# Optimization experiments

Hardware: AMD Instinct MI355X
Metric: run time of the kernel (lower is better)

Reference implementation:

```python
import jax, jax.numpy as jnp
import numpy as np

B = 256        # graph pairs
MAX_SET = 64   # nodes per graph == max_set_size (padding is identity)
E = 512        # edges per graph
D = 128        # node_state_dim == av.filters_3
T = 64         # av.transform_dim
N_PROP = 5
N_TIME = 3
TEMP = 0.1
SINK_ITERS = 20
NG = 2 * B
N = NG * MAX_SET
TOT_E = NG * E


def sinkhorn(log_alpha):
    la = log_alpha / TEMP
    for _ in range(SINK_ITERS):
        la = la - jax.nn.logsumexp(la, axis=2, keepdims=True)
        la = la - jax.nn.logsumexp(la, axis=1, keepdims=True)
    return jnp.exp(la)


def setup_inputs() -> dict:
    key = jax.random.key(0)
    ks = jax.random.split(key, 32)

    def lin(k, i, o):
        return jax.random.normal(k, (i, o), jnp.float32) / np.sqrt(i).astype(np.float32)

    node_features = jax.random.normal(ks[0], (N, 32), jnp.float32)
    edge_features = jax.random.normal(ks[1], (TOT_E, 16), jnp.float32)
    offs = jnp.repeat(jnp.arange(NG, dtype=jnp.int32) * MAX_SET, E)
    from_idx = jax.random.randint(ks[2], (TOT_E,), 0, MAX_SET, jnp.int32) + offs
    to_idx = jax.random.randint(ks[3], (TOT_E,), 0, MAX_SET, jnp.int32) + offs
    return {
        "node_features": node_features, "edge_features": edge_features,
        "from_idx": from_idx, "to_idx": to_idx,
        "node_enc_w": lin(ks[4], 32, D), "node_enc_b": jnp.zeros((D,), jnp.float32),
        "edge_enc_w": lin(ks[5], 16, 64), "edge_enc_b": jnp.zeros((64,), jnp.float32),
        "mw1": lin(ks[6], 2 * D + 64, 2 * D), "mb1": jnp.zeros((2 * D,), jnp.float32),
        "mw2": lin(ks[7], 2 * D, D), "mb2": jnp.zeros((D,), jnp.float32),
        "nw1": lin(ks[8], 2 * D, 2 * D), "nb1": jnp.zeros((2 * D,), jnp.float32),
        "nw2": lin(ks[9], 2 * D, D), "nb2": jnp.zeros((D,), jnp.float32),
        "cw1": lin(ks[10], 2 * D, 2 * D), "cb1": jnp.zeros((2 * D,), jnp.float32),
        "cw2": lin(ks[11], 2 * D, D), "cb2": jnp.zeros((D,), jnp.float32),
        "t1w": lin(ks[12], D, T), "t1b": jnp.zeros((T,), jnp.float32),
        "t2w": lin(ks[13], T, T), "t2b": jnp.zeros((T,), jnp.float32),
    }


def reference(node_features, edge_features, from_idx, to_idx,
              node_enc_w, node_enc_b, edge_enc_w, edge_enc_b,
              mw1, mb1, mw2, mb2, nw1, nb1, nw2, nb2,
              cw1, cb1, cw2, cb2, t1w, t1b, t2w, t2b):
    # Encoder (GMN GraphEncoder: linear maps on raw node/edge features)
    h0 = node_features @ node_enc_w + node_enc_b          # [N, D]
    e0 = edge_features @ edge_enc_w + edge_enc_b          # [TOT_E, 64]
    store = jnp.zeros((N, D * (N_PROP + 1)), h0.dtype)    # node_feature_store
    plan = None
    for _t in range(N_TIME):
        h = h0
        parts = [jnp.zeros((N, D), h0.dtype)]             # slot 0 stays zero
        for p in range(1, N_PROP + 1):
            inter = store[:, (p - 1) * D: p * D]          # time_update_idx == 'k_t'
            comb = jax.nn.relu(jnp.concatenate([h, inter], 1) @ cw1 + cb1) @ cw2 + cb2
            # GraphPropLayer: gather -> message MLP -> segment_sum -> node update MLP
            msg_in = jnp.concatenate([comb[from_idx], comb[to_idx], e0], 1)
            messages = jax.nn.relu(msg_in @ mw1 + mb1) @ mw2 + mb2
            agg = jax.ops.segment_sum(messages, to_idx, num_segments=N)
            h = jax.nn.relu(jnp.concatenate([comb, agg], 1) @ nw1 + nb1) @ nw2 + nb2
            parts.append(h)
        store = jnp.concatenate(parts, 1)                 # [N, D*(K+1)]
        # split into padded query/corpus stacks (all graphs have MAX_SET nodes,
        # so F.pad and the size masks are identity here)
        s = store.reshape(NG, MAX_SET, -1)
        q, c = s[0::2], s[1::2]                           # [B, M, D*(K+1)]
        tq = jax.nn.relu(q[:, :, -D:] @ t1w + t1b) @ t2w + t2b
        tc = jax.nn.relu(c[:, :, -D:] @ t1w + t1b) @ t2w + t2b
        sim = jnp.einsum('bqt,bct->bqc', tq, tc)
        plan = sinkhorn(sim)                              # node transport plan [B,M,M]
        qfc = jnp.einsum('bqc,bcd->bqd', plan, c)
        cfq = jnp.einsum('bqc,bqd->bcd', plan, q)
        inter_feats = jnp.stack([qfc, cfq], 1)[:, :, :, D:].reshape(N, N_PROP * D)
        store = store.at[:, D:].set(inter_feats)
    return plan
```

## Files before the change

kernel.cpp:

```cpp
#include <hip/hip_runtime.h>
#include <hip/hip_bf16.h>

#define NNODES   32768
#define NGROUPS  512
#define EPG      512
#define ND       (32768l*128)

typedef __attribute__((ext_vector_type(4))) float f32x4;
typedef __attribute__((ext_vector_type(8))) short bf16x8;

__device__ __forceinline__ short f2bf(float x) {
  unsigned u = __float_as_uint(x);
  unsigned r = (u + 0x7FFF + ((u >> 16) & 1)) >> 16;
  return (short)r;
}
__device__ __forceinline__ float bf2f(short h) {
  return __uint_as_float(((unsigned)(unsigned short)h) << 16);
}
__device__ __forceinline__ void split3(float x, short* ph, short* pm, short* pl, long idx) {
  short h = f2bf(x); float r1 = x - bf2f(h);
  short m = f2bf(r1); float r2 = r1 - bf2f(m);
  ph[idx] = h; pm[idx] = m; pl[idx] = f2bf(r2);
}

__global__ void k_node_enc(const float* __restrict__ nf, const float* __restrict__ w,
                           const float* __restrict__ b, float* __restrict__ h0) {
  int idx = blockIdx.x * 256 + threadIdx.x;
  int row = idx >> 7, col = idx & 127;
  const float* x = nf + row * 32;
  float acc = b[col];
#pragma unroll
  for (int k = 0; k < 32; ++k) acc = fmaf(x[k], w[k * 128 + col], acc);
  h0[idx] = acc;
}

__global__ void k_prep(const float* __restrict__ eew, const float* __restrict__ eeb,
                       const float* __restrict__ mw1, const float* __restrict__ mb1,
                       const float* __restrict__ mb2, const float* __restrict__ nw1,
                       float* __restrict__ Wfold, float* __restrict__ bfold,
                       float* __restrict__ vbias) {
  const int c = threadIdx.x, b = blockIdx.x;
  if (b < 16) {
    float a = 0.f;
    for (int j = 0; j < 64; ++j) a = fmaf(eew[b * 64 + j], mw1[(256 + j) * 256 + c], a);
    Wfold[b * 256 + c] = a;
  } else if (b == 16) {
    float a = mb1[c];
    for (int j = 0; j < 64; ++j) a = fmaf(eeb[j], mw1[(256 + j) * 256 + c], a);
    bfold[c] = a;
  } else {
    float a = 0.f;
    for (int j = 0; j < 128; ++j) a = fmaf(mb2[j], nw1[(128 + j) * 256 + c], a);
    vbias[c] = a;
  }
}

__global__ void k_wsplit3(const float* __restrict__ W, int C, int Kd,
                          short* __restrict__ th, short* __restrict__ tm,
                          short* __restrict__ tl) {
  const int c = blockIdx.x;
  for (int k = threadIdx.x; k < Kd; k += 256) {
    float w = W[(long)k * C + c];
    split3(w, th, tm, tl, c * 256 + k);
  }
}

__global__ void k_csr(const int* __restrict__ from_idx, const int* __restrict__ to_idx,
                      const float* __restrict__ ef,
                      int* __restrict__ csr_f, int* __restrict__ rp_g,
                      float* __restrict__ efp, int* __restrict__ deg) {
  __shared__ int cnt[64], rps[65];
  __shared__ int tls[EPG], fls[EPG];
  __shared__ short ord[EPG];
  const int g = blockIdx.x, tid = threadIdx.x;
  const int be = g * EPG, bn = g * 64;
  if (tid < 64) cnt[tid] = 0;
  __syncthreads();
  for (int e = tid; e < EPG; e += 256) {
    int t = to_idx[be + e] - bn;
    tls[e] = t;
    fls[e] = from_idx[be + e] - bn;
    atomicAdd(&cnt[t], 1);
  }
  __syncthreads();
  if (tid == 0) {
    int s = 0;
    for (int i = 0; i < 64; ++i) { rps[i] = s; s += cnt[i]; }
    rps[64] = s;
  }
  __syncthreads();
  if (tid < 64) {
    int pos = rps[tid];
    for (int e = 0; e < EPG; ++e)
      if (tls[e] == tid) ord[pos++] = (short)e;
  }
  __syncthreads();
  for (int ec = tid; ec < EPG; ec += 256) {
    const int eo = ord[ec];
    csr_f[be + ec] = fls[eo];
    const float4* src = (const float4*)&ef[(long)(be + eo) * 16];
    float4* dst = (float4*)&efp[(long)(be + ec) * 16];
    dst[0] = src[0]; dst[1] = src[1]; dst[2] = src[2]; dst[3] = src[3];
  }
  if (tid < 65) rp_g[g * 65 + tid] = rps[tid];
  if (tid < 64) deg[bn + tid] = cnt[tid];
}

template<int KTOT, bool DEG, bool RPX0, bool WPOUT>
__global__ __launch_bounds__(256, 3)
void k_mlp2m(const float* __restrict__ x0,
             const short* __restrict__ x0h, const short* __restrict__ x0m,
             const short* __restrict__ x0l,
             const float* __restrict__ x1,
             const short* __restrict__ W1h, const short* __restrict__ W1m,
             const short* __restrict__ W1l,
             const float* __restrict__ b1, const int* __restrict__ deg,
             const float* __restrict__ vbias,
             const short* __restrict__ W2h, const short* __restrict__ W2m,
             const short* __restrict__ W2l,
             const float* __restrict__ b2,
             float* __restrict__ out,
             short* __restrict__ outh, short* __restrict__ outm,
             short* __restrict__ outl) {
  __shared__ short xh[32 * 264];
  __shared__ short xm[32 * 264];
  __shared__ short xl[32 * 264];
  __shared__ int degs[32];
  const int tid = threadIdx.x;
  const long row0 = (long)blockIdx.x * 32;

  if constexpr (RPX0) {
    for (int i = tid; i < 32 * 16; i += 256) {
      const int r = i >> 4, q = i & 15;
      const long gb = (row0 + r) * 128 + q * 8;
      const int lb = r * 264 + q * 8;
      *(bf16x8*)&xh[lb] = *(const bf16x8*)&x0h[gb];
      *(bf16x8*)&xm[lb] = *(const bf16x8*)&x0m[gb];
      *(bf16x8*)&xl[lb] = *(const bf16x8*)&x0l[gb];
    }
  } else {
    for (int i = tid; i < 32 * 32; i += 256) {
      const int r = i >> 5, q = i & 31;
      float4 v = *(const float4*)&x0[(row0 + r) * 128 + q * 4];
      const int base = r * 264 + q * 4;
      split3(v.x, xh, xm, xl, base + 0);
      split3(v.y, xh, xm, xl, base + 1);
      split3(v.z, xh, xm, xl, base + 2);
      split3(v.w, xh, xm, xl, base + 3);
    }
  }
  if constexpr (KTOT == 256) {
    for (int i = tid; i < 32 * 32; i += 256) {
      const int r = i >> 5, q = i & 31;
      float4 v = *(const float4*)&x1[(row0 + r) * 128 + q * 4];
      const int base = r * 264 + 128 + q * 4;
      split3(v.x, xh, xm, xl, base + 0);
      split3(v.y, xh, xm, xl, base + 1);
      split3(v.z, xh, xm, xl, base + 2);
      split3(v.w, xh, xm, xl, base + 3);
    }
  }
  if constexpr (DEG) { if (tid < 32) degs[tid] = deg[row0 + tid]; }
  __syncthreads();

  const int lane = tid & 63, wid = tid >> 6;
  const int lr = lane & 15;
  const int lk = (lane >> 4) * 8;
  const int rsub = (lane >> 4) * 4;

  f32x4 acc[2][4];
#pragma unroll
  for (int fc = 0; fc < 4; ++fc) {
    const int col = wid * 64 + fc * 16 + lr;
    const float bv = b1[col];
#pragma unroll
    for (int fr = 0; fr < 2; ++fr) acc[fr][fc] = {bv, bv, bv, bv};
    if constexpr (DEG) {
      const float vb = vbias[col];
#pragma unroll
      for (int fr = 0; fr < 2; ++fr)
#pragma unroll
        for (int r = 0; r < 4; ++r)
          acc[fr][fc][r] += (float)degs[fr * 16 + rsub + r] * vb;
    }
  }

#pragma unroll 2
  for (int ks = 0; ks < KTOT / 32; ++ks) {
    const int k0 = ks * 32 + lk;
    bf16x8 ah[2], am[2], al[2];
#pragma unroll
    for (int fr = 0; fr < 2; ++fr) {
      const int ab = (fr * 16 + lr) * 264 + k0;
      ah[fr] = *(const bf16x8*)&xh[ab];
      am[fr] = *(const bf16x8*)&xm[ab];
      al[fr] = *(const bf16x8*)&xl[ab];
    }
#pragma unroll
    for (int fc = 0; fc < 4; ++fc) {
      const long wrow = (long)(wid * 64 + fc * 16 + lr) * 256 + k0;
      const bf16x8 bh = *(const bf16x8*)&W1h[wrow];
      const bf16x8 bm = *(const bf16x8*)&W1m[wrow];
      const bf16x8 bl = *(const bf16x8*)&W1l[wrow];
#pragma unroll
      for (int fr = 0; fr < 2; ++fr) {
        acc[fr][fc] = __builtin_amdgcn_mfma_f32_16x16x32_bf16(ah[fr], bh, acc[fr][fc], 0, 0, 0);
        acc[fr][fc] = __builtin_amdgcn_mfma_f32_16x16x32_bf16(ah[fr], bm, acc[fr][fc], 0, 0, 0);
        acc[fr][fc] = __builtin_amdgcn_mfma_f32_16x16x32_bf16(am[fr], bh, acc[fr][fc], 0, 0, 0);
        acc[fr][fc] = __builtin_amdgcn_mfma_f32_16x16x32_bf16(ah[fr], bl, acc[fr][fc], 0, 0, 0);
        acc[fr][fc] = __builtin_amdgcn_mfma_f32_16x16x32_bf16(am[fr], bm, acc[fr][fc], 0, 0, 0);
        acc[fr][fc] = __builtin_amdgcn_mfma_f32_16x16x32_bf16(al[fr], bh, acc[fr][fc], 0, 0, 0);
      }
    }
  }
  __syncthreads();

#pragma unroll
  for (int fr = 0; fr < 2; ++fr)
#pragma unroll
    for (int fc = 0; fc < 4; ++fc) {
      const int col = wid * 64 + fc * 16 + lr;
#pragma unroll
      for (int r = 0; r < 4; ++r) {
        const int row = fr * 16 + rsub + r;
        float v = fmaxf(acc[fr][fc][r], 0.f);
        split3(v, xh, xm, xl, row * 264 + col);
      }
    }
  __syncthreads();

  f32x4 acc2[2][2];
#pragma unroll
  for (int fc = 0; fc < 2; ++fc) {
    const float bv = b2[wid * 32 + fc * 16 + lr];
#pragma unroll
    for (int fr = 0; fr < 2; ++fr) acc2[fr][fc] = {bv, bv, bv, bv};
  }
#pragma unroll 2
  for (int ks = 0; ks < 8; ++ks) {
    const int k0 = ks * 32 + lk;
    bf16x8 ah[2], am[2], al[2];
#pragma unroll
    for (int fr = 0; fr < 2; ++fr) {
      const int ab = (fr * 16 + lr) * 264 + k0;
      ah[fr] = *(const bf16x8*)&xh[ab];
      am[fr] = *(const bf16x8*)&xm[ab];
      al[fr] = *(const bf16x8*)&xl[ab];
    }
#pragma unroll
    for (int fc = 0; fc < 2; ++fc) {
      const long wrow = (long)(wid * 32 + fc * 16 + lr) * 256 + k0;
      const bf16x8 bh = *(const bf16x8*)&W2h[wrow];
      const bf16x8 bm = *(const bf16x8*)&W2m[wrow];
      const bf16x8 bl = *(const bf16x8*)&W2l[wrow];
#pragma unroll
      for (int fr = 0; fr < 2; ++fr) {
        acc2[fr][fc] = __builtin_amdgcn_mfma_f32_16x16x32_bf16(ah[fr], bh, acc2[fr][fc], 0, 0, 0);
        acc2[fr][fc] = __builtin_amdgcn_mfma_f32_16x16x32_bf16(ah[fr], bm, acc2[fr][fc], 0, 0, 0);
        acc2[fr][fc] = __builtin_amdgcn_mfma_f32_16x16x32_bf16(am[fr], bh, acc2[fr][fc], 0, 0, 0);
        acc2[fr][fc] = __builtin_amdgcn_mfma_f32_16x16x32_bf16(ah[fr], bl, acc2[fr][fc], 0, 0, 0);
        acc2[fr][fc] = __builtin_amdgcn_mfma_f32_16x16x32_bf16(am[fr], bm, acc2[fr][fc], 0, 0, 0);
        acc2[fr][fc] = __builtin_amdgcn_mfma_f32_16x16x32_bf16(al[fr], bh, acc2[fr][fc], 0, 0, 0);
      }
    }
  }
#pragma unroll
  for (int fr = 0; fr < 2; ++fr)
#pragma unroll
    for (int fc = 0; fc < 2; ++fc) {
      const int col = wid * 32 + fc * 16 + lr;
#pragma unroll
      for (int r = 0; r < 4; ++r) {
        const long gi = (row0 + fr * 16 + rsub + r) * 128 + col;
        if constexpr (WPOUT) {
          split3(acc2[fr][fc][r], outh, outm, outl, gi);
        } else {
          out[gi] = acc2[fr][fc][r];
        }
      }
    }
}

__global__ __launch_bounds__(256, 3)
void k_edgeb(const short* __restrict__ chp, const short* __restrict__ cmp,
             const short* __restrict__ clp,
             const float* __restrict__ efp,
             const short* __restrict__ m1h, const short* __restrict__ m1m,
             const short* __restrict__ m1l,
             const float* __restrict__ Wfold, const float* __restrict__ bfold,
             const int* __restrict__ csr_f, const int* __restrict__ rp_g,
             float* __restrict__ ag) {
  __shared__ __align__(16) float cAB[2 * 64 * 68];
  __shared__ short fl[EPG];
  __shared__ int rp[65];
  float* cA = cAB;
  float* cB = cAB + 64 * 68;

  const int tid = threadIdx.x;
  const int g = blockIdx.x, cb = blockIdx.y;
  const int be = g * EPG, bn = g * 64;
  const int col0 = cb * 64;

  for (int i = tid; i < EPG; i += 256) fl[i] = (short)csr_f[be + i];
  if (tid < 65) rp[tid] = rp_g[g * 65 + tid];

  const int lane = tid & 63, wid = tid >> 6;
  const int lr = lane & 15;
  const int lk = (lane >> 4) * 8;
  const int rsub = (lane >> 4) * 4;
  const int ng = tid >> 4, cg = tid & 15;
  const int n0 = ng * 4, cq = cg * 4;

  {
    const int isB = wid >> 1;
    const int cw = (wid & 1) * 32;
    const int wkof = isB * 128;
    float* dstC = isB ? cB : cA;
#pragma unroll 1
    for (int hf = 0; hf < 2; ++hf) {
      f32x4 c[2][2];
#pragma unroll
      for (int fr = 0; fr < 2; ++fr)
#pragma unroll
        for (int fc = 0; fc < 2; ++fc) c[fr][fc] = {0.f, 0.f, 0.f, 0.f};
      for (int ks = 0; ks < 4; ++ks) {
        const int k0 = ks * 32 + lk;
        bf16x8 ah[2], am[2], al[2];
#pragma unroll
        for (int fr = 0; fr < 2; ++fr) {
          const long ga = (long)(bn + (hf * 2 + fr) * 16 + lr) * 128 + k0;
          ah[fr] = *(const bf16x8*)&chp[ga];
          am[fr] = *(const bf16x8*)&cmp[ga];
          al[fr] = *(const bf16x8*)&clp[ga];
        }
#pragma unroll
        for (int fc = 0; fc < 2; ++fc) {
          const long wrow = (long)(col0 + cw + fc * 16 + lr) * 256 + wkof + k0;
          const bf16x8 bh = *(const bf16x8*)&m1h[wrow];
          const bf16x8 bm = *(const bf16x8*)&m1m[wrow];
          const bf16x8 bl = *(const bf16x8*)&m1l[wrow];
#pragma unroll
          for (int fr = 0; fr < 2; ++fr) {
            c[fr][fc] = __builtin_amdgcn_mfma_f32_16x16x32_bf16(ah[fr], bh, c[fr][fc], 0, 0, 0);
            c[fr][fc] = __builtin_amdgcn_mfma_f32_16x16x32_bf16(ah[fr], bm, c[fr][fc], 0, 0, 0);
            c[fr][fc] = __builtin_amdgcn_mfma_f32_16x16x32_bf16(am[fr], bh, c[fr][fc], 0, 0, 0);
            c[fr][fc] = __builtin_amdgcn_mfma_f32_16x16x32_bf16(ah[fr], bl, c[fr][fc], 0, 0, 0);
            c[fr][fc] = __builtin_amdgcn_mfma_f32_16x16x32_bf16(am[fr], bm, c[fr][fc], 0, 0, 0);
            c[fr][fc] = __builtin_amdgcn_mfma_f32_16x16x32_bf16(al[fr], bh, c[fr][fc], 0, 0, 0);
          }
        }
      }
#pragma unroll
      for (int fr = 0; fr < 2; ++fr)
#pragma unroll
        for (int fc = 0; fc < 2; ++fc) {
          const int col = cw + fc * 16 + lr;
#pragma unroll
          for (int r = 0; r < 4; ++r)
            dstC[((hf * 2 + fr) * 16 + rsub + r) * 68 + col] = c[fr][fc][r];
        }
    }
  }
  float4 Wf[16];
#pragma unroll
  for (int k = 0; k < 16; ++k) Wf[k] = *(const float4*)&Wfold[k * 256 + col0 + cq];
  const float4 bf = *(const float4*)&bfold[col0 + cq];
  __syncthreads();

#pragma unroll
  for (int i = 0; i < 4; ++i) {
    const int n = n0 + i;
    const float4 cBn = *(const float4*)&cB[n * 68 + cq];
    const int eBeg = rp[n], eEnd = rp[n + 1];
    float4 acc0 = make_float4(0.f, 0.f, 0.f, 0.f);
    float4 acc1 = make_float4(0.f, 0.f, 0.f, 0.f);
    int e = eBeg;
    for (; e + 1 < eEnd; e += 2) {
      const int f0 = fl[e], f1 = fl[e + 1];
      const float* er0 = efp + (long)(be + e) * 16;
      const float* er1 = efp + (long)(be + e + 1) * 16;
      float4 ea[4], eb[4];
#pragma unroll
      for (int kq = 0; kq < 4; ++kq) { ea[kq] = ((const float4*)er0)[kq]; eb[kq] = ((const float4*)er1)[kq]; }
      float4 h0 = bf, h1 = bf;
#pragma unroll
      for (int kq = 0; kq < 4; ++kq) {
        const float ev0[4] = {ea[kq].x, ea[kq].y, ea[kq].z, ea[kq].w};
        const float ev1[4] = {eb[kq].x, eb[kq].y, eb[kq].z, eb[kq].w};
#pragma unroll
        for (int s = 0; s < 4; ++s) {
          const float4 w = Wf[kq * 4 + s];
          h0.x = fmaf(ev0[s], w.x, h0.x); h0.y = fmaf(ev0[s], w.y, h0.y);
          h0.z = fmaf(ev0[s], w.z, h0.z); h0.w = fmaf(ev0[s], w.w, h0.w);
          h1.x = fmaf(ev1[s], w.x, h1.x); h1.y = fmaf(ev1[s], w.y, h1.y);
          h1.z = fmaf(ev1[s], w.z, h1.z); h1.w = fmaf(ev1[s], w.w, h1.w);
        }
      }
      const float4 va0 = *(const float4*)&cA[f0 * 68 + cq];
      const float4 va1 = *(const float4*)&cA[f1 * 68 + cq];
      acc0.x += fmaxf(h0.x + va0.x + cBn.x, 0.f);
      acc0.y += fmaxf(h0.y + va0.y + cBn.y, 0.f);
      acc0.z += fmaxf(h0.z + va0.z + cBn.z, 0.f);
      acc0.w += fmaxf(h0.w + va0.w + cBn.w, 0.f);
      acc1.x += fmaxf(h1.x + va1.x + cBn.x, 0.f);
      acc1.y += fmaxf(h1.y + va1.y + cBn.y, 0.f);
      acc1.z += fmaxf(h1.z + va1.z + cBn.z, 0.f);
      acc1.w += fmaxf(h1.w + va1.w + cBn.w, 0.f);
    }
    if (e < eEnd) {
      const int f = fl[e];
      const float* er = efp + (long)(be + e) * 16;
      float4 h = bf;
#pragma unroll
      for (int kq = 0; kq < 4; ++kq) {
        const float4 e4 = ((const float4*)er)[kq];
        const float ev[4] = {e4.x, e4.y, e4.z, e4.w};
#pragma unroll
        for (int s = 0; s < 4; ++s) {
          const float4 w = Wf[kq * 4 + s];
          h.x = fmaf(ev[s], w.x, h.x); h.y = fmaf(ev[s], w.y, h.y);
          h.z = fmaf(ev[s], w.z, h.z); h.w = fmaf(ev[s], w.w, h.w);
        }
      }
      const float4 va = *(const float4*)&cA[f * 68 + cq];
      acc0.x += fmaxf(h.x + va.x + cBn.x, 0.f);
      acc0.y += fmaxf(h.y + va.y + cBn.y, 0.f);
      acc0.z += fmaxf(h.z + va.z + cBn.z, 0.f);
      acc0.w += fmaxf(h.w + va.w + cBn.w, 0.f);
    }
    acc0.x += acc1.x; acc0.y += acc1.y; acc0.z += acc1.z; acc0.w += acc1.w;
    *(float4*)&ag[(long)(bn + n) * 256 + col0 + cq] = acc0;
  }
}

__global__ __launch_bounds__(256, 3)
void k_aggm(const float* __restrict__ ag,
            const short* __restrict__ m2h, const short* __restrict__ m2m,
            const short* __restrict__ m2l, float* __restrict__ aggM) {
  __shared__ short xh[32 * 264];
  __shared__ short xm[32 * 264];
  __shared__ short xl[32 * 264];
  const int tid = threadIdx.x;
  const long row0 = (long)blockIdx.x * 32;

  for (int i = tid; i < 2048; i += 256) {
    const int r = i >> 6, q = i & 63;
    float4 v = *(const float4*)&ag[(row0 + r) * 256 + q * 4];
    const int base = r * 264 + q * 4;
    split3(v.x, xh, xm, xl, base + 0);
    split3(v.y, xh, xm, xl, base + 1);
    split3(v.z, xh, xm, xl, base + 2);
    split3(v.w, xh, xm, xl, base + 3);
  }
  __syncthreads();

  const int lane = tid & 63, wid = tid >> 6;
  const int lr = lane & 15;
  const int lk = (lane >> 4) * 8;
  const int rsub = (lane >> 4) * 4;

  f32x4 s0[2][2], s1[2][2];
#pragma unroll
  for (int fc = 0; fc < 2; ++fc)
#pragma unroll
    for (int fr = 0; fr < 2; ++fr) { s0[fr][fc] = {0.f, 0.f, 0.f, 0.f}; s1[fr][fc] = {0.f, 0.f, 0.f, 0.f}; }

#pragma unroll 2
  for (int ks = 0; ks < 4; ++ks) {
    const int k0 = ks * 32 + lk;
    bf16x8 ah[2], am[2], al[2];
#pragma unroll
    for (int fr = 0; fr < 2; ++fr) {
      const int ab = (fr * 16 + lr) * 264 + k0;
      ah[fr] = *(const bf16x8*)&xh[ab];
      am[fr] = *(const bf16x8*)&xm[ab];
      al[fr] = *(const bf16x8*)&xl[ab];
    }
#pragma unroll
    for (int fc = 0; fc < 2; ++fc) {
      const long wrow = (long)(wid * 32 + fc * 16 + lr) * 256 + k0;
      const bf16x8 bh = *(const bf16x8*)&m2h[wrow];
      const bf16x8 bm = *(const bf16x8*)&m2m[wrow];
      const bf16x8 bl = *(const bf16x8*)&m2l[wrow];
#pragma unroll
      for (int fr = 0; fr < 2; ++fr) {
        s0[fr][fc] = __builtin_amdgcn_mfma_f32_16x16x32_bf16(ah[fr], bh, s0[fr][fc], 0, 0, 0);
        s0[fr][fc] = __builtin_amdgcn_mfma_f32_16x16x32_bf16(ah[fr], bm, s0[fr][fc], 0, 0, 0);
        s0[fr][fc] = __builtin_amdgcn_mfma_f32_16x16x32_bf16(am[fr], bh, s0[fr][fc], 0, 0, 0);
        s0[fr][fc] = __builtin_amdgcn_mfma_f32_16x16x32_bf16(ah[fr], bl, s0[fr][fc], 0, 0, 0);
        s0[fr][fc] = __builtin_amdgcn_mfma_f32_16x16x32_bf16(am[fr], bm, s0[fr][fc], 0, 0, 0);
        s0[fr][fc] = __builtin_amdgcn_mfma_f32_16x16x32_bf16(al[fr], bh, s0[fr][fc], 0, 0, 0);
      }
    }
  }
#pragma unroll 2
  for (int ks = 4; ks < 8; ++ks) {
    const int k0 = ks * 32 + lk;
    bf16x8 ah[2], am[2], al[2];
#pragma unroll
    for (int fr = 0; fr < 2; ++fr) {
      const int ab = (fr * 16 + lr) * 264 + k0;
      ah[fr] = *(const bf16x8*)&xh[ab];
      am[fr] = *(const bf16x8*)&xm[ab];
      al[fr] = *(const bf16x8*)&xl[ab];
    }
#pragma unroll
    for (int fc = 0; fc < 2; ++fc) {
      const long wrow = (long)(wid * 32 + fc * 16 + lr) * 256 + k0;
      const bf16x8 bh = *(const bf16x8*)&m2h[wrow];
      const bf16x8 bm = *(const bf16x8*)&m2m[wrow];
      const bf16x8 bl = *(const bf16x8*)&m2l[wrow];
#pragma unroll
      for (int fr = 0; fr < 2; ++fr) {
        s1[fr][fc] = __builtin_amdgcn_mfma_f32_16x16x32_bf16(ah[fr], bh, s1[fr][fc], 0, 0, 0);
        s1[fr][fc] = __builtin_amdgcn_mfma_f32_16x16x32_bf16(ah[fr], bm, s1[fr][fc], 0, 0, 0);
        s1[fr][fc] = __builtin_amdgcn_mfma_f32_16x16x32_bf16(am[fr], bh, s1[fr][fc], 0, 0, 0);
        s1[fr][fc] = __builtin_amdgcn_mfma_f32_16x16x32_bf16(ah[fr], bl, s1[fr][fc], 0, 0, 0);
        s1[fr][fc] = __builtin_amdgcn_mfma_f32_16x16x32_bf16(am[fr], bm, s1[fr][fc], 0, 0, 0);
        s1[fr][fc] = __builtin_amdgcn_mfma_f32_16x16x32_bf16(al[fr], bh, s1[fr][fc], 0, 0, 0);
      }
    }
  }
#pragma unroll
  for (int fr = 0; fr < 2; ++fr)
#pragma unroll
    for (int fc = 0; fc < 2; ++fc) {
      const int col = wid * 32 + fc * 16 + lr;
#pragma unroll
      for (int r = 0; r < 4; ++r)
        aggM[(row0 + fr * 16 + rsub + r) * 128 + col] = s0[fr][fc][r] + s1[fr][fc][r];
    }
}

__global__ void k_tfeat(const float* __restrict__ x,
                        const float* __restrict__ t1w, const float* __restrict__ t1b,
                        const float* __restrict__ t2w, const float* __restrict__ t2b,
                        float* __restrict__ tf) {
  __shared__ float xs[4][128];
  __shared__ float ys[4][64];
  const int tid = threadIdx.x;
  const long row0 = (long)blockIdx.x * 4;
  for (int i = tid; i < 512; i += 256)
    xs[i >> 7][i & 127] = x[(row0 + (i >> 7)) * 128 + (i & 127)];
  __syncthreads();
  const int r = tid >> 6, c = tid & 63;
  float acc = t1b[c];
#pragma unroll 4
  for (int k = 0; k < 128; ++k) acc = fmaf(xs[r][k], t1w[k * 64 + c], acc);
  ys[r][c] = fmaxf(acc, 0.f);
  __syncthreads();
  float a2 = t2b[c];
#pragma unroll 4
  for (int k = 0; k < 64; ++k) a2 = fmaf(ys[r][k], t2w[k * 64 + c], a2);
  tf[(row0 + r) * 64 + c] = a2;
}

__global__ void k_sim(const float* __restrict__ tf, float* __restrict__ sim) {
  const int b = blockIdx.x, tid = threadIdx.x;
  __shared__ float tq[64][65];
  __shared__ float tcs[64][65];
  for (int i = tid; i < 4096; i += 256) {
    tq[i >> 6][i & 63]  = tf[(long)b * 8192 + i];
    tcs[i >> 6][i & 63] = tf[(long)b * 8192 + 4096 + i];
  }
  __syncthreads();
  const int m = tid >> 2, j0 = (tid & 3) * 16;
#pragma unroll
  for (int j = 0; j < 16; ++j) {
    float a = 0.f;
#pragma unroll 4
    for (int k = 0; k < 64; ++k) a = fmaf(tq[m][k], tcs[j0 + j][k], a);
    sim[(long)b * 4096 + m * 64 + j0 + j] = a;
  }
}

__global__ void k_sink(float* __restrict__ sim, float* __restrict__ outp) {
  const int b = blockIdx.x, tid = threadIdx.x;
  __shared__ float la[64][65];
  const float C = 14.426950408889634f;
  for (int i = tid; i < 4096; i += 256)
    la[i >> 6][i & 63] = sim[(long)b * 4096 + i] * C;
  __syncthreads();
  const int r4 = tid >> 2, l4 = tid & 3;
  for (int it = 0; it < 20; ++it) {
    {
      float m = -3.4e38f;
#pragma unroll
      for (int i = 0; i < 16; ++i) m = fmaxf(m, la[r4][l4 + 4 * i]);
      m = fmaxf(m, __shfl_xor(m, 1)); m = fmaxf(m, __shfl_xor(m, 2));
      float s = 0.f;
#pragma unroll
      for (int i = 0; i < 16; ++i) s += exp2f(la[r4][l4 + 4 * i] - m);
      s += __shfl_xor(s, 1); s += __shfl_xor(s, 2);
      const float lse = m + log2f(s);
#pragma unroll
      for (int i = 0; i < 16; ++i) la[r4][l4 + 4 * i] -= lse;
    }
    __syncthreads();
    {
      float m = -3.4e38f;
#pragma unroll
      for (int i = 0; i < 16; ++i) m = fmaxf(m, la[l4 + 4 * i][r4]);
      m = fmaxf(m, __shfl_xor(m, 1)); m = fmaxf(m, __shfl_xor(m, 2));
      float s = 0.f;
#pragma unroll
      for (int i = 0; i < 16; ++i) s += exp2f(la[l4 + 4 * i][r4] - m);
      s += __shfl_xor(s, 1); s += __shfl_xor(s, 2);
      const float lse = m + log2f(s);
#pragma unroll
      for (int i = 0; i < 16; ++i) la[l4 + 4 * i][r4] -= lse;
    }
    __syncthreads();
  }
  for (int i = tid; i < 4096; i += 256) {
    const float v = exp2f(la[i >> 6][i & 63]);
    outp[(long)b * 4096 + i] = v;
    sim[(long)b * 4096 + i] = v;
  }
}

__global__ void k_mix(const float* __restrict__ plan, const float* __restrict__ src,
                      float* __restrict__ dst) {
  const int b = blockIdx.x, tid = threadIdx.x;
  __shared__ float pl[64][65];
  __shared__ float qs[64][128];
  __shared__ float cs[64][128];
  const long qbase = (long)(2 * b) * 64, cbase = qbase + 64;
  for (int i = tid; i < 4096; i += 256) pl[i >> 6][i & 63] = plan[(long)b * 4096 + i];
  for (int i = tid; i < 8192; i += 256) {
    qs[i >> 7][i & 127] = src[qbase * 128 + i];
    cs[i >> 7][i & 127] = src[cbase * 128 + i];
  }
  __syncthreads();
  const int d = tid & 127, m0 = (tid >> 7) * 32;
  for (int m = m0; m < m0 + 32; ++m) {
    float a = 0.f;
#pragma unroll 4
    for (int j = 0; j < 64; ++j) a = fmaf(pl[m][j], cs[j][d], a);
    dst[(qbase + m) * 128 + d] = a;
  }
  for (int j = m0; j < m0 + 32; ++j) {
    float a = 0.f;
#pragma unroll 4
    for (int m = 0; m < 64; ++m) a = fmaf(pl[m][j], qs[m][d], a);
    dst[(cbase + j) * 128 + d] = a;
  }
}

extern "C" void kernel_launch(void* const* d_in, const int* in_sizes, int n_in,
                              void* d_out, int out_size, void* d_ws, size_t ws_size,
                              hipStream_t stream) {
  const float* nf  = (const float*)d_in[0];
  const float* ef  = (const float*)d_in[1];
  const int* from_idx = (const int*)d_in[2];
  const int* to_idx   = (const int*)d_in[3];
  const float* new_w = (const float*)d_in[4];
  const float* new_b = (const float*)d_in[5];
  const float* eew = (const float*)d_in[6];
  const float* eeb = (const float*)d_in[7];
  const float* mw1 = (const float*)d_in[8];
  const float* mb1 = (const float*)d_in[9];
  const float* mw2 = (const float*)d_in[10];
  const float* mb2 = (const float*)d_in[11];
  const float* nw1 = (const float*)d_in[12];
  const float* nb1 = (const float*)d_in[13];
  const float* nw2 = (const float*)d_in[14];
  const float* nb2 = (const float*)d_in[15];
  const float* cw1 = (const float*)d_in[16];
  const float* cb1 = (const float*)d_in[17];
  const float* cw2 = (const float*)d_in[18];
  const float* cb2 = (const float*)d_in[19];
  const float* t1w = (const float*)d_in[20];
  const float* t1b = (const float*)d_in[21];
  const float* t2w = (const float*)d_in[22];
  const float* t2b = (const float*)d_in[23];

  float* W = (float*)d_ws;
  float* h0     = W;
  float* aggM0  = h0 + ND;
  float* ag     = aggM0 + ND;
  float* parts  = ag + 2 * ND;
  float* efp    = parts + 5 * ND;
  float* Wfold  = efp + 262144l * 16;
  float* bfold  = Wfold + 4096;
  float* vbias  = bfold + 256;
  int*   deg    = (int*)(vbias + 256);
  int*   csr_f  = deg + 32768;
  int*   rp_g   = csr_f + 262144;
  short* cw1t_h = (short*)(rp_g + 33280);
  short* cw1t_m = cw1t_h + 65536;
  short* cw1t_l = cw1t_m + 65536;
  short* nw1t_h = cw1t_l + 65536;
  short* nw1t_m = nw1t_h + 65536;
  short* nw1t_l = nw1t_m + 65536;
  short* cw2t_h = nw1t_l + 65536;
  short* cw2t_m = cw2t_h + 32768;
  short* cw2t_l = cw2t_m + 32768;
  short* nw2t_h = cw2t_l + 32768;
  short* nw2t_m = nw2t_h + 32768;
  short* nw2t_l = nw2t_m + 32768;
  short* m1t_h  = nw2t_l + 32768;
  short* m1t_m  = m1t_h + 65536;
  short* m1t_l  = m1t_m + 65536;
  short* m2t_h  = m1t_l + 65536;
  short* m2t_m  = m2t_h + 32768;
  short* m2t_l  = m2t_m + 32768;
  short* chp    = m2t_l + 32768;
  short* cmp    = chp + 32768l * 128;
  short* clp    = cmp + 32768l * 128;
  float* tf     = aggM0;
  float* sim    = aggM0 + 2097152;
  float* outp   = (float*)d_out;

  k_prep<<<18, 256, 0, stream>>>(eew, eeb, mw1, mb1, mb2, nw1, Wfold, bfold, vbias);
  k_csr<<<512, 256, 0, stream>>>(from_idx, to_idx, ef, csr_f, rp_g, efp, deg);
  k_wsplit3<<<256, 256, 0, stream>>>(cw1, 256, 256, cw1t_h, cw1t_m, cw1t_l);
  k_wsplit3<<<256, 256, 0, stream>>>(nw1, 256, 256, nw1t_h, nw1t_m, nw1t_l);
  k_wsplit3<<<128, 256, 0, stream>>>(cw2, 128, 256, cw2t_h, cw2t_m, cw2t_l);
  k_wsplit3<<<128, 256, 0, stream>>>(nw2, 128, 256, nw2t_h, nw2t_m, nw2t_l);
  k_wsplit3<<<256, 256, 0, stream>>>(mw1, 256, 256, m1t_h, m1t_m, m1t_l);
  k_wsplit3<<<128, 256, 0, stream>>>(mw2, 128, 256, m2t_h, m2t_m, m2t_l);
  k_node_enc<<<16384, 256, 0, stream>>>(nf, new_w, new_b, h0);

  for (int t = 0; t < 3; ++t) {
    const float* hprev = h0;
    for (int p = 1; p <= 5; ++p) {
      if (t > 0 && p > 1)
        k_mlp2m<256, false, false, true><<<1024, 256, 0, stream>>>(
            hprev, nullptr, nullptr, nullptr,
            parts + (long)(p - 1) * ND,
            cw1t_h, cw1t_m, cw1t_l, cb1, nullptr, nullptr,
            cw2t_h, cw2t_m, cw2t_l, cb2, nullptr, chp, cmp, clp);
      else
        k_mlp2m<128, false, false, true><<<1024, 256, 0, stream>>>(
            hprev, nullptr, nullptr, nullptr, nullptr,
            cw1t_h, cw1t_m, cw1t_l, cb1, nullptr, nullptr,
            cw2t_h, cw2t_m, cw2t_l, cb2, nullptr, chp, cmp, clp);
      k_edgeb<<<dim3(512, 4), 256, 0, stream>>>(chp, cmp, clp, efp,
                                                m1t_h, m1t_m, m1t_l,
                                                Wfold, bfold, csr_f, rp_g, ag);
      k_aggm<<<1024, 256, 0, stream>>>(ag, m2t_h, m2t_m, m2t_l, aggM0);
      float* hnew = parts + (long)(p - 1) * ND;
      k_mlp2m<256, true, true, false><<<1024, 256, 0, stream>>>(
          nullptr, chp, cmp, clp, aggM0,
          nw1t_h, nw1t_m, nw1t_l, nb1, deg, vbias,
          nw2t_h, nw2t_m, nw2t_l, nb2, hnew, nullptr, nullptr, nullptr);
      hprev = hnew;
    }
    k_tfeat<<<8192, 256, 0, stream>>>(parts + 4 * ND, t1w, t1b, t2w, t2b, tf);
    k_sim<<<256, 256, 0, stream>>>(tf, sim);
    k_sink<<<256, 256, 0, stream>>>(sim, outp);
    if (t < 2) {
      for (int pi = 3; pi >= 0; --pi)
        k_mix<<<256, 256, 0, stream>>>(sim, parts + (long)pi * ND, parts + (long)(pi + 1) * ND);
    }
  }
}
```

Before: 5.611 ms.

## Fuse message-aggregate projection into node-update MLP kernel and unroll edge loop by three

The separate k_aggm kernel, which projected the aggregated message sums through mw2, is removed. That projection now runs as a prologue inside the node-update k_mlp2m, whose result is split straight into the shared-memory operand tiles. This drops one launch per propagation step and the global write and read of the 128-wide aggM buffer. Separately, the edge accumulation loop in k_edgeb is unrolled by three instead of two, which adds ILP but raises register pressure; the fused kernel also uses more registers and runs longer per block.

```diff
diff --git a/kernel.cpp b/kernel.cpp
--- a/kernel.cpp
+++ b/kernel.cpp
@@ -106,12 +106,14 @@
   if (tid < 64) deg[bn + tid] = cnt[tid];
 }
 
-template<int KTOT, bool DEG, bool RPX0, bool WPOUT>
+template<int KTOT, bool DEG, bool RPX0, bool WPOUT, bool AGG>
 __global__ __launch_bounds__(256, 3)
 void k_mlp2m(const float* __restrict__ x0,
              const short* __restrict__ x0h, const short* __restrict__ x0m,
              const short* __restrict__ x0l,
              const float* __restrict__ x1,
+             const short* __restrict__ A2h, const short* __restrict__ A2m,
+             const short* __restrict__ A2l,
              const short* __restrict__ W1h, const short* __restrict__ W1m,
              const short* __restrict__ W1l,
              const float* __restrict__ b1, const int* __restrict__ deg,
@@ -129,6 +131,100 @@
   const int tid = threadIdx.x;
   const long row0 = (long)blockIdx.x * 32;
 
+  const int lane = tid & 63, wid = tid >> 6;
+  const int lr = lane & 15;
+  const int lk = (lane >> 4) * 8;
+  const int rsub = (lane >> 4) * 4;
+
+  if constexpr (AGG) {
+    for (int i = tid; i < 2048; i += 256) {
+      const int r = i >> 6, q = i & 63;
+      float4 v = *(const float4*)&x1[(row0 + r) * 256 + q * 4];
+      const int base = r * 264 + q * 4;
+      split3(v.x, xh, xm, xl, base + 0);
+      split3(v.y, xh, xm, xl, base + 1);
+      split3(v.z, xh, xm, xl, base + 2);
+      split3(v.w, xh, xm, xl, base + 3);
+    }
+    __syncthreads();
+
+    f32x4 s0[2][2], s1[2][2];
+#pragma unroll
+    for (int fc = 0; fc < 2; ++fc)
+#pragma unroll
+      for (int fr = 0; fr < 2; ++fr) { s0[fr][fc] = {0.f,0.f,0.f,0.f}; s1[fr][fc] = {0.f,0.f,0.f,0.f}; }
+
+#pragma unroll 2
+    for (int ks = 0; ks < 4; ++ks) {
+      const int k0 = ks * 32 + lk;
+      bf16x8 ah[2], am[2], al[2];
+#pragma unroll
+      for (int fr = 0; fr < 2; ++fr) {
+        const int ab = (fr * 16 + lr) * 264 + k0;
+        ah[fr] = *(const bf16x8*)&xh[ab];
+        am[fr] = *(const bf16x8*)&xm[ab];
+        al[fr] = *(const bf16x8*)&xl[ab];
+      }
+#pragma unroll
+      for (int fc = 0; fc < 2; ++fc) {
+        const long wrow = (long)(wid * 32 + fc * 16 + lr) * 256 + k0;
+        const bf16x8 bh = *(const bf16x8*)&A2h[wrow];
+        const bf16x8 bm = *(const bf16x8*)&A2m[wrow];
+        const bf16x8 bl = *(const bf16x8*)&A2l[wrow];
+#pragma unroll
+        for (int fr = 0; fr < 2; ++fr) {
+          s0[fr][fc] = __builtin_amdgcn_mfma_f32_16x16x32_bf16(ah[fr], bh, s0[fr][fc], 0, 0, 0);
+          s0[fr][fc] = __builtin_amdgcn_mfma_f32_16x16x32_bf16(ah[fr], bm, s0[fr][fc], 0, 0, 0);
+          s0[fr][fc] = __builtin_amdgcn_mfma_f32_16x16x32_bf16(am[fr], bh, s0[fr][fc], 0, 0, 0);
+          s0[fr][fc] = __builtin_amdgcn_mfma_f32_16x16x32_bf16(ah[fr], bl, s0[fr][fc], 0, 0, 0);
+          s0[fr][fc] = __builtin_amdgcn_mfma_f32_16x16x32_bf16(am[fr], bm, s0[fr][fc], 0, 0, 0);
+          s0[fr][fc] = __builtin_amdgcn_mfma_f32_16x16x32_bf16(al[fr], bh, s0[fr][fc], 0, 0, 0);
+        }
+      }
+    }
+#pragma unroll 2
+    for (int ks = 4; ks < 8; ++ks) {
+      const int k0 = ks * 32 + lk;
+      bf16x8 ah[2], am[2], al[2];
+#pragma unroll
+      for (int fr = 0; fr < 2; ++fr) {
+        const int ab = (fr * 16 + lr) * 264 + k0;
+        ah[fr] = *(const bf16x8*)&xh[ab];
+        am[fr] = *(const bf16x8*)&xm[ab];
+        al[fr] = *(const bf16x8*)&xl[ab];
+      }
+#pragma unroll
+      for (int fc = 0; fc < 2; ++fc) {
+        const long wrow = (long)(wid * 32 + fc * 16 + lr) * 256 + k0;
+        const bf16x8 bh = *(const bf16x8*)&A2h[wrow];
+        const bf16x8 bm = *(const bf16x8*)&A2m[wrow];
+        const bf16x8 bl = *(const bf16x8*)&A2l[wrow];
+#pragma unroll
+        for (int fr = 0; fr < 2; ++fr) {
+          s1[fr][fc] = __builtin_amdgcn_mfma_f32_16x16x32_bf16(ah[fr], bh, s1[fr][fc], 0, 0, 0);
+          s1[fr][fc] = __builtin_amdgcn_mfma_f32_16x16x32_bf16(ah[fr], bm, s1[fr][fc], 0, 0, 0);
+          s1[fr][fc] = __builtin_amdgcn_mfma_f32_16x16x32_bf16(am[fr], bh, s1[fr][fc], 0, 0, 0);
+          s1[fr][fc] = __builtin_amdgcn_mfma_f32_16x16x32_bf16(ah[fr], bl, s1[fr][fc], 0, 0, 0);
+          s1[fr][fc] = __builtin_amdgcn_mfma_f32_16x16x32_bf16(am[fr], bm, s1[fr][fc], 0, 0, 0);
+          s1[fr][fc] = __builtin_amdgcn_mfma_f32_16x16x32_bf16(al[fr], bh, s1[fr][fc], 0, 0, 0);
+        }
+      }
+    }
+    __syncthreads();
+
+#pragma unroll
+    for (int fr = 0; fr < 2; ++fr)
+#pragma unroll
+      for (int fc = 0; fc < 2; ++fc) {
+        const int col = wid * 32 + fc * 16 + lr;
+#pragma unroll
+        for (int r = 0; r < 4; ++r) {
+          const int row = fr * 16 + rsub + r;
+          split3(s0[fr][fc][r] + s1[fr][fc][r], xh, xm, xl, row * 264 + 128 + col);
+        }
+      }
+  }
+
   if constexpr (RPX0) {
     for (int i = tid; i < 32 * 16; i += 256) {
       const int r = i >> 4, q = i & 15;
@@ -149,7 +245,7 @@
       split3(v.w, xh, xm, xl, base + 3);
     }
   }
-  if constexpr (KTOT == 256) {
+  if constexpr (KTOT == 256 && !AGG) {
     for (int i = tid; i < 32 * 32; i += 256) {
       const int r = i >> 5, q = i & 31;
       float4 v = *(const float4*)&x1[(row0 + r) * 128 + q * 4];
@@ -162,11 +258,6 @@
   }
   if constexpr (DEG) { if (tid < 32) degs[tid] = deg[row0 + tid]; }
   __syncthreads();
-
-  const int lane = tid & 63, wid = tid >> 6;
-  const int lr = lane & 15;
-  const int lk = (lane >> 4) * 8;
-  const int rsub = (lane >> 4) * 4;
 
   f32x4 acc[2][4];
 #pragma unroll
@@ -371,22 +462,29 @@
   for (int i = 0; i < 4; ++i) {
     const int n = n0 + i;
     const float4 cBn = *(const float4*)&cB[n * 68 + cq];
-    const int eBeg = rp[n], eEnd = rp[n + 1];
-    float4 acc0 = make_float4(0.f, 0.f, 0.f, 0.f);
-    float4 acc1 = make_float4(0.f, 0.f, 0.f, 0.f);
-    int e = eBeg;
-    for (; e + 1 < eEnd; e += 2) {
-      const int f0 = fl[e], f1 = fl[e + 1];
+    const int eEnd = rp[n + 1];
+    float4 a0 = make_float4(0.f, 0.f, 0.f, 0.f);
+    float4 a1 = make_float4(0.f, 0.f, 0.f, 0.f);
+    float4 a2 = make_float4(0.f, 0.f, 0.f, 0.f);
+    int e = rp[n];
+    for (; e + 2 < eEnd; e += 3) {
+      const int f0 = fl[e], f1 = fl[e + 1], f2 = fl[e + 2];
       const float* er0 = efp + (long)(be + e) * 16;
       const float* er1 = efp + (long)(be + e + 1) * 16;
-      float4 ea[4], eb[4];
-#pragma unroll
-      for (int kq = 0; kq < 4; ++kq) { ea[kq] = ((const float4*)er0)[kq]; eb[kq] = ((const float4*)er1)[kq]; }
-      float4 h0 = bf, h1 = bf;
+      const float* er2 = efp + (long)(be + e + 2) * 16;
+      float4 ea[4], eb[4], ec[4];
+#pragma unroll
+      for (int kq = 0; kq < 4; ++kq) {
+        ea[kq] = ((const float4*)er0)[kq];
+        eb[kq] = ((const float4*)er1)[kq];
+        ec[kq] = ((const float4*)er2)[kq];
+      }
+      float4 h0 = bf, h1 = bf, h2 = bf;
 #pragma unroll
       for (int kq = 0; kq < 4; ++kq) {
         const float ev0[4] = {ea[kq].x, ea[kq].y, ea[kq].z, ea[kq].w};
         const float ev1[4] = {eb[kq].x, eb[kq].y, eb[kq].z, eb[kq].w};
+        const float ev2[4] = {ec[kq].x, ec[kq].y, ec[kq].z, ec[kq].w};
 #pragma unroll
         for (int s = 0; s < 4; ++s) {
           const float4 w = Wf[kq * 4 + s];
@@ -394,20 +492,27 @@
           h0.z = fmaf(ev0[s], w.z, h0.z); h0.w = fmaf(ev0[s], w.w, h0.w);
           h1.x = fmaf(ev1[s], w.x, h1.x); h1.y = fmaf(ev1[s], w.y, h1.y);
           h1.z = fmaf(ev1[s], w.z, h1.z); h1.w = fmaf(ev1[s], w.w, h1.w);
+          h2.x = fmaf(ev2[s], w.x, h2.x); h2.y = fmaf(ev2[s], w.y, h2.y);
+          h2.z = fmaf(ev2[s], w.z, h2.z); h2.w = fmaf(ev2[s], w.w, h2.w);
         }
       }
       const float4 va0 = *(const float4*)&cA[f0 * 68 + cq];
       const float4 va1 = *(const float4*)&cA[f1 * 68 + cq];
-      acc0.x += fmaxf(h0.x + va0.x + cBn.x, 0.f);
-      acc0.y += fmaxf(h0.y + va0.y + cBn.y, 0.f);
-      acc0.z += fmaxf(h0.z + va0.z + cBn.z, 0.f);
-      acc0.w += fmaxf(h0.w + va0.w + cBn.w, 0.f);
-      acc1.x += fmaxf(h1.x + va1.x + cBn.x, 0.f);
-      acc1.y += fmaxf(h1.y + va1.y + cBn.y, 0.f);
-      acc1.z += fmaxf(h1.z + va1.z + cBn.z, 0.f);
-      acc1.w += fmaxf(h1.w + va1.w + cBn.w, 0.f);
-    }
-    if (e < eEnd) {
+      const float4 va2 = *(const float4*)&cA[f2 * 68 + cq];
+      a0.x += fmaxf(h0.x + va0.x + cBn.x, 0.f);
+      a0.y += fmaxf(h0.y + va0.y + cBn.y, 0.f);
+      a0.z += fmaxf(h0.z + va0.z + cBn.z, 0.f);
+      a0.w += fmaxf(h0.w + va0.w + cBn.w, 0.f);
+      a1.x += fmaxf(h1.x + va1.x + cBn.x, 0.f);
+      a1.y += fmaxf(h1.y + va1.y + cBn.y, 0.f);
+      a1.z += fmaxf(h1.z + va1.z + cBn.z, 0.f);
+      a1.w += fmaxf(h1.w + va1.w + cBn.w, 0.f);
+      a2.x += fmaxf(h2.x + va2.x + cBn.x, 0.f);
+      a2.y += fmaxf(h2.y + va2.y + cBn.y, 0.f);
+      a2.z += fmaxf(h2.z + va2.z + cBn.z, 0.f);
+      a2.w += fmaxf(h2.w + va2.w + cBn.w, 0.f);
+    }
+    for (; e < eEnd; ++e) {
       const int f = fl[e];
       const float* er = efp + (long)(be + e) * 16;
       float4 h = bf;
@@ -423,113 +528,15 @@
         }
       }
       const float4 va = *(const float4*)&cA[f * 68 + cq];
-      acc0.x += fmaxf(h.x + va.x + cBn.x, 0.f);
-      acc0.y += fmaxf(h.y + va.y + cBn.y, 0.f);
-      acc0.z += fmaxf(h.z + va.z + cBn.z, 0.f);
-      acc0.w += fmaxf(h.w + va.w + cBn.w, 0.f);
-    }
-    acc0.x += acc1.x; acc0.y += acc1.y; acc0.z += acc1.z; acc0.w += acc1.w;
-    *(float4*)&ag[(long)(bn + n) * 256 + col0 + cq] = acc0;
-  }
-}
-
-__global__ __launch_bounds__(256, 3)
-void k_aggm(const float* __restrict__ ag,
-            const short* __restrict__ m2h, const short* __restrict__ m2m,
-            const short* __restrict__ m2l, float* __restrict__ aggM) {
-  __shared__ short xh[32 * 264];
-  __shared__ short xm[32 * 264];
-  __shared__ short xl[32 * 264];
-  const int tid = threadIdx.x;
-  const long row0 = (long)blockIdx.x * 32;
-
-  for (int i = tid; i < 2048; i += 256) {
-    const int r = i >> 6, q = i & 63;
-    float4 v = *(const float4*)&ag[(row0 + r) * 256 + q * 4];
-    const int base = r * 264 + q * 4;
-    split3(v.x, xh, xm, xl, base + 0);
-    split3(v.y, xh, xm, xl, base + 1);
-    split3(v.z, xh, xm, xl, base + 2);
-    split3(v.w, xh, xm, xl, base + 3);
-  }
-  __syncthreads();
-
-  const int lane = tid & 63, wid = tid >> 6;
-  const int lr = lane & 15;
-  const int lk = (lane >> 4) * 8;
-  const int rsub = (lane >> 4) * 4;
-
-  f32x4 s0[2][2], s1[2][2];
-#pragma unroll
-  for (int fc = 0; fc < 2; ++fc)
-#pragma unroll
-    for (int fr = 0; fr < 2; ++fr) { s0[fr][fc] = {0.f, 0.f, 0.f, 0.f}; s1[fr][fc] = {0.f, 0.f, 0.f, 0.f}; }
-
-#pragma unroll 2
-  for (int ks = 0; ks < 4; ++ks) {
-    const int k0 = ks * 32 + lk;
-    bf16x8 ah[2], am[2], al[2];
-#pragma unroll
-    for (int fr = 0; fr < 2; ++fr) {
-      const int ab = (fr * 16 + lr) * 264 + k0;
-      ah[fr] = *(const bf16x8*)&xh[ab];
-      am[fr] = *(const bf16x8*)&xm[ab];
-      al[fr] = *(const bf16x8*)&xl[ab];
-    }
-#pragma unroll
-    for (int fc = 0; fc < 2; ++fc) {
-      const long wrow = (long)(wid * 32 + fc * 16 + lr) * 256 + k0;
-      const bf16x8 bh = *(const bf16x8*)&m2h[wrow];
-      const bf16x8 bm = *(const bf16x8*)&m2m[wrow];
-      const bf16x8 bl = *(const bf16x8*)&m2l[wrow];
-#pragma unroll
-      for (int fr = 0; fr < 2; ++fr) {
-        s0[fr][fc] = __builtin_amdgcn_mfma_f32_16x16x32_bf16(ah[fr], bh, s0[fr][fc], 0, 0, 0);
-        s0[fr][fc] = __builtin_amdgcn_mfma_f32_16x16x32_bf16(ah[fr], bm, s0[fr][fc], 0, 0, 0);
-        s0[fr][fc] = __builtin_amdgcn_mfma_f32_16x16x32_bf16(am[fr], bh, s0[fr][fc], 0, 0, 0);
-        s0[fr][fc] = __builtin_amdgcn_mfma_f32_16x16x32_bf16(ah[fr], bl, s0[fr][fc], 0, 0, 0);
-        s0[fr][fc] = __builtin_amdgcn_mfma_f32_16x16x32_bf16(am[fr], bm, s0[fr][fc], 0, 0, 0);
-        s0[fr][fc] = __builtin_amdgcn_mfma_f32_16x16x32_bf16(al[fr], bh, s0[fr][fc], 0, 0, 0);
-      }
-    }
-  }
-#pragma unroll 2
-  for (int ks = 4; ks < 8; ++ks) {
-    const int k0 = ks * 32 + lk;
-    bf16x8 ah[2], am[2], al[2];
-#pragma unroll
-    for (int fr = 0; fr < 2; ++fr) {
-      const int ab = (fr * 16 + lr) * 264 + k0;
-      ah[fr] = *(const bf16x8*)&xh[ab];
-      am[fr] = *(const bf16x8*)&xm[ab];
-      al[fr] = *(const bf16x8*)&xl[ab];
-    }
-#pragma unroll
-    for (int fc = 0; fc < 2; ++fc) {
-      const long wrow = (long)(wid * 32 + fc * 16 + lr) * 256 + k0;
-      const bf16x8 bh = *(const bf16x8*)&m2h[wrow];
-      const bf16x8 bm = *(const bf16x8*)&m2m[wrow];
-      const bf16x8 bl = *(const bf16x8*)&m2l[wrow];
-#pragma unroll
-      for (int fr = 0; fr < 2; ++fr) {
-        s1[fr][fc] = __builtin_amdgcn_mfma_f32_16x16x32_bf16(ah[fr], bh, s1[fr][fc], 0, 0, 0);
-        s1[fr][fc] = __builtin_amdgcn_mfma_f32_16x16x32_bf16(ah[fr], bm, s1[fr][fc], 0, 0, 0);
-        s1[fr][fc] = __builtin_amdgcn_mfma_f32_16x16x32_bf16(am[fr], bh, s1[fr][fc], 0, 0, 0);
-        s1[fr][fc] = __builtin_amdgcn_mfma_f32_16x16x32_bf16(ah[fr], bl, s1[fr][fc], 0, 0, 0);
-        s1[fr][fc] = __builtin_amdgcn_mfma_f32_16x16x32_bf16(am[fr], bm, s1[fr][fc], 0, 0, 0);
-        s1[fr][fc] = __builtin_amdgcn_mfma_f32_16x16x32_bf16(al[fr], bh, s1[fr][fc], 0, 0, 0);
-      }
-    }
-  }
-#pragma unroll
-  for (int fr = 0; fr < 2; ++fr)
-#pragma unroll
-    for (int fc = 0; fc < 2; ++fc) {
-      const int col = wid * 32 + fc * 16 + lr;
-#pragma unroll
-      for (int r = 0; r < 4; ++r)
-        aggM[(row0 + fr * 16 + rsub + r) * 128 + col] = s0[fr][fc][r] + s1[fr][fc][r];
-    }
+      a0.x += fmaxf(h.x + va.x + cBn.x, 0.f);
+      a0.y += fmaxf(h.y + va.y + cBn.y, 0.f);
+      a0.z += fmaxf(h.z + va.z + cBn.z, 0.f);
+      a0.w += fmaxf(h.w + va.w + cBn.w, 0.f);
+    }
+    a0.x += a1.x; a0.y += a1.y; a0.z += a1.z; a0.w += a1.w;
+    a0.x += a2.x; a0.y += a2.y; a0.z += a2.z; a0.w += a2.w;
+    *(float4*)&ag[(long)(bn + n) * 256 + col0 + cq] = a0;
+  }
 }
 
 __global__ void k_tfeat(const float* __restrict__ x,
@@ -726,23 +733,22 @@
     const float* hprev = h0;
     for (int p = 1; p <= 5; ++p) {
       if (t > 0 && p > 1)
-        k_mlp2m<256, false, false, true><<<1024, 256, 0, stream>>>(
+        k_mlp2m<256, false, false, true, false><<<1024, 256, 0, stream>>>(
             hprev, nullptr, nullptr, nullptr,
-            parts + (long)(p - 1) * ND,
+            parts + (long)(p - 1) * ND, nullptr, nullptr, nullptr,
             cw1t_h, cw1t_m, cw1t_l, cb1, nullptr, nullptr,
             cw2t_h, cw2t_m, cw2t_l, cb2, nullptr, chp, cmp, clp);
       else
-        k_mlp2m<128, false, false, true><<<1024, 256, 0, stream>>>(
-            hprev, nullptr, nullptr, nullptr, nullptr,
+        k_mlp2m<128, false, false, true, false><<<1024, 256, 0, stream>>>(
+            hprev, nullptr, nullptr, nullptr, nullptr, nullptr, nullptr, nullptr,
             cw1t_h, cw1t_m, cw1t_l, cb1, nullptr, nullptr,
             cw2t_h, cw2t_m, cw2t_l, cb2, nullptr, chp, cmp, clp);
       k_edgeb<<<dim3(512, 4), 256, 0, stream>>>(chp, cmp, clp, efp,
                                                 m1t_h, m1t_m, m1t_l,
                                                 Wfold, bfold, csr_f, rp_g, ag);
-      k_aggm<<<1024, 256, 0, stream>>>(ag, m2t_h, m2t_m, m2t_l, aggM0);
       float* hnew = parts + (long)(p - 1) * ND;
-      k_mlp2m<256, true, true, false><<<1024, 256, 0, stream>>>(
-          nullptr, chp, cmp, clp, aggM0,
+      k_mlp2m<256, true, true, false, true><<<1024, 256, 0, stream>>>(
+          nullptr, chp, cmp, clp, ag, m2t_h, m2t_m, m2t_l,
           nw1t_h, nw1t_m, nw1t_l, nb1, deg, vbias,
           nw2t_h, nw2t_m, nw2t_l, nb2, hnew, nullptr, nullptr, nullptr);
       hprev = hnew;
```

Result: no change. 5.539 ms (-1.3%).
